# Optimization experiments

Measured on AMD Instinct MI355X. Metric: run time of the kernel, lower is better.

## Reference

```python
import jax, jax.numpy as jnp
import numpy as np

# Qwen3-Next gated delta-net dims
H_K, H_V, DK, DV = 16, 32, 128, 128
HID, KCONV = 2048, 4
KEY_DIM, VALUE_DIM = H_K * DK, H_V * DV      # 2048, 4096
CONV_DIM = 2 * KEY_DIM + VALUE_DIM           # 8192
GV = H_V // H_K                              # v-heads per k-head = 2
EPS = 1e-6
SEQ = 4096


def setup_inputs() -> dict:
    key = jax.random.key(0)
    ks = jax.random.split(key, 8)
    n = lambda k, sh, s: jax.random.normal(k, sh, jnp.float32) * s
    return {
        "hidden_states": n(ks[0], (SEQ, HID), 1.0),
        "W_qkvz": n(ks[1], (HID, 2 * KEY_DIM + 2 * VALUE_DIM), HID ** -0.5),
        "W_ba": n(ks[2], (HID, 2 * H_V), HID ** -0.5),
        "conv_w": n(ks[3], (CONV_DIM, KCONV), 0.5),
        "A_log": jnp.log(jax.random.uniform(ks[4], (H_V,), jnp.float32, 1.0, 16.0)),
        "dt_bias": jnp.ones((H_V,), jnp.float32),
        "norm_weight": jnp.ones((DV,), jnp.float32),
        "W_out": n(ks[5], (VALUE_DIM, HID), VALUE_DIM ** -0.5),
    }


def _l2norm(x):
    return x * jax.lax.rsqrt(jnp.sum(x * x, -1, keepdims=True) + EPS)


def reference(hidden_states, W_qkvz, W_ba, conv_w, A_log, dt_bias, norm_weight, W_out):
    L = hidden_states.shape[0]
    # 1. input projections
    qkvz = hidden_states @ W_qkvz            # (L, 12288)
    ba = hidden_states @ W_ba                # (L, 64)
    # fix_query_key_value_ordering: view per k-head group then split
    qkvz = qkvz.reshape(L, H_K, 2 * DK + 2 * GV * DV)
    q = qkvz[:, :, :DK]                                         # (L, Hk, dk)
    k = qkvz[:, :, DK:2 * DK]                                   # (L, Hk, dk)
    v = qkvz[:, :, 2 * DK:2 * DK + GV * DV].reshape(L, H_V, DV)  # (L, Hv, dv)
    z = qkvz[:, :, 2 * DK + GV * DV:].reshape(L, H_V, DV)
    ba = ba.reshape(L, H_K, 2 * GV)
    b = ba[:, :, :GV].reshape(L, H_V)
    a = ba[:, :, GV:].reshape(L, H_V)

    # 2. causal depthwise conv1d over [q|k|v] channels + silu
    mixed = jnp.concatenate([q.reshape(L, KEY_DIM), k.reshape(L, KEY_DIM),
                             v.reshape(L, VALUE_DIM)], axis=-1)  # (L, CONV_DIM)
    xp = jnp.pad(mixed, ((KCONV - 1, 0), (0, 0)))
    conv = sum(xp[i:i + L] * conv_w[:, i] for i in range(KCONV))
    mixed = jax.nn.silu(conv)

    q = mixed[:, :KEY_DIM].reshape(L, H_K, DK)
    k = mixed[:, KEY_DIM:2 * KEY_DIM].reshape(L, H_K, DK)
    v = mixed[:, 2 * KEY_DIM:].reshape(L, H_V, DV)

    # 3. fused gating: g = -exp(A_log) * softplus(a + dt_bias); beta = sigmoid(b)
    g = -jnp.exp(A_log) * jax.nn.softplus(a + dt_bias)   # (L, Hv)
    beta = jax.nn.sigmoid(b)                              # (L, Hv)

    # qk l2-norm + scale, expand k-heads to v-heads (GQA repeat)
    q = jnp.repeat(_l2norm(q), GV, axis=1) * (DK ** -0.5)  # (L, Hv, dk)
    k = jnp.repeat(_l2norm(k), GV, axis=1)

    # 4. gated delta-rule recurrence over time (state per head: dk x dv)
    def step(S, inp):
        qt, kt, vt, gt, bt = inp
        S = S * jnp.exp(gt)[:, None, None]
        kv = jnp.einsum('hkv,hk->hv', S, kt)
        delta = (vt - kv) * bt[:, None]
        S = S + kt[:, :, None] * delta[:, None, :]
        return S, jnp.einsum('hkv,hk->hv', S, qt)

    S0 = jnp.zeros((H_V, DK, DV), jnp.float32)
    _, core = jax.lax.scan(step, S0, (q, k, v, g, beta))   # (L, Hv, dv)

    # 5. gated RMSNorm (norm before gate): rmsnorm(x)*w * silu(z)
    var = jnp.mean(core * core, -1, keepdims=True)
    core = core * jax.lax.rsqrt(var + EPS) * norm_weight
    core = core * jax.nn.silu(z)

    # 6. output projection
    return core.reshape(L, VALUE_DIM) @ W_out
```

## Files before the change

### kernel.cpp

```cpp
#include <hip/hip_runtime.h>
#include <hip/hip_bf16.h>

#define SEQ 4096
#define HID 2048
#define HK_ 16
#define HV_ 32
#define KEY_DIM 2048
#define VALUE_DIM 4096
#define CONV_DIM 8192
#define NQKVZ 12288

typedef unsigned short ushort_t;
typedef short bf16x8 __attribute__((ext_vector_type(8)));
typedef float f32x4 __attribute__((ext_vector_type(4)));
typedef float f32x2 __attribute__((ext_vector_type(2)));

__device__ __forceinline__ float bf2f(ushort_t h) {
    union { unsigned int u; float f; } x; x.u = ((unsigned int)h) << 16; return x.f;
}
__device__ __forceinline__ void cvt8(uint4 v, float* f) {
    unsigned int w[4] = {v.x, v.y, v.z, v.w};
#pragma unroll
    for (int i = 0; i < 4; i++) {
        union { unsigned int u; float f; } lo, hi;
        lo.u = w[i] << 16; hi.u = w[i] & 0xffff0000u;
        f[2 * i] = lo.f; f[2 * i + 1] = hi.f;
    }
}
__device__ __forceinline__ void cvt8v(uint4 v, f32x2* f) {
    unsigned int w[4] = {v.x, v.y, v.z, v.w};
#pragma unroll
    for (int i = 0; i < 4; i++) {
        union { unsigned int u; float f; } lo, hi;
        lo.u = w[i] << 16; hi.u = w[i] & 0xffff0000u;
        f[i] = (f32x2){lo.f, hi.f};
    }
}
__device__ __forceinline__ ushort_t f2bf(float f) {
    union { float f; unsigned int u; } x; x.f = f;
    unsigned int u = x.u;
    u += 0x7fffu + ((u >> 16) & 1u);
    return (ushort_t)(u >> 16);
}

template <int CTRL>
__device__ __forceinline__ float dpp_add(float x) {
    union { float f; int i; } a, b;
    a.f = x;
    b.i = __builtin_amdgcn_update_dpp(0, a.i, CTRL, 0xF, 0xF, true);
    return a.f + b.f;
}
__device__ __forceinline__ float red16(float x) {
    x = dpp_add<0xB1>(x);
    x = dpp_add<0x4E>(x);
    x = dpp_add<0x141>(x);
    x = dpp_add<0x140>(x);
    return x;
}

__global__ void k_cvt(const float* __restrict__ src, ushort_t* __restrict__ dst)
{
    size_t i = ((size_t)blockIdx.x * 256 + threadIdx.x) * 8;
    float4 a = *(const float4*)&src[i];
    float4 b = *(const float4*)&src[i + 4];
    ushort_t u[8];
    u[0]=f2bf(a.x); u[1]=f2bf(a.y); u[2]=f2bf(a.z); u[3]=f2bf(a.w);
    u[4]=f2bf(b.x); u[5]=f2bf(b.y); u[6]=f2bf(b.z); u[7]=f2bf(b.w);
    *(uint4*)&dst[i] = *(uint4*)u;
}

__global__ __launch_bounds__(256) void k_transpose(const float* __restrict__ src,
                                                   ushort_t* __restrict__ dst,
                                                   int R, int C)
{
    __shared__ float tile[64][65];
    int c0 = blockIdx.x * 64, r0 = blockIdx.y * 64;
    int t = threadIdx.x;
    int tr = t >> 4, tc = (t & 15) * 4;
#pragma unroll
    for (int r = 0; r < 4; r++) {
        float4 v = *(const float4*)&src[(size_t)(r0 + tr + r * 16) * C + c0 + tc];
        tile[tr + r * 16][tc + 0] = v.x;
        tile[tr + r * 16][tc + 1] = v.y;
        tile[tr + r * 16][tc + 2] = v.z;
        tile[tr + r * 16][tc + 3] = v.w;
    }
    __syncthreads();
#pragma unroll
    for (int r = 0; r < 4; r++) {
        int n = c0 + tr + r * 16;
        ushort_t u[4];
#pragma unroll
        for (int i = 0; i < 4; i++) u[i] = f2bf(tile[tc + i][tr + r * 16]);
        *(uint2*)&dst[(size_t)n * R + r0 + tc] = *(uint2*)u;
    }
}

__global__ void k_ba(const float* __restrict__ A, const float* __restrict__ B,
                     const float* __restrict__ A_log, const float* __restrict__ dt_bias,
                     float* __restrict__ gbf)
{
    __shared__ float As[16][132];
    __shared__ float Bs[16][68];
    int tid = threadIdx.x;
    int m0 = blockIdx.x * 128;
    int tx = tid & 15, ty = tid >> 4;
    int arow = tid >> 2, akq = tid & 3;
    int brow = tid >> 4, bc4 = tid & 15;
    float acc[8][4];
#pragma unroll
    for (int i = 0; i < 8; i++)
#pragma unroll
        for (int j = 0; j < 4; j++) acc[i][j] = 0.f;

    for (int k0 = 0; k0 < HID; k0 += 16) {
        float4 a0 = *(const float4*)&A[(size_t)(m0 + arow) * HID + k0 + akq * 4];
        float4 a1 = *(const float4*)&A[(size_t)(m0 + arow + 64) * HID + k0 + akq * 4];
        float4 b0 = *(const float4*)&B[(size_t)(k0 + brow) * 64 + bc4 * 4];
        __syncthreads();
        As[akq * 4 + 0][arow] = a0.x; As[akq * 4 + 1][arow] = a0.y;
        As[akq * 4 + 2][arow] = a0.z; As[akq * 4 + 3][arow] = a0.w;
        As[akq * 4 + 0][arow + 64] = a1.x; As[akq * 4 + 1][arow + 64] = a1.y;
        As[akq * 4 + 2][arow + 64] = a1.z; As[akq * 4 + 3][arow + 64] = a1.w;
        *(float4*)&Bs[brow][bc4 * 4] = b0;
        __syncthreads();
#pragma unroll
        for (int kk = 0; kk < 16; kk++) {
            float xa[8], yb[4];
            *(float4*)&xa[0] = *(const float4*)&As[kk][ty * 8];
            *(float4*)&xa[4] = *(const float4*)&As[kk][ty * 8 + 4];
            *(float4*)&yb[0] = *(const float4*)&Bs[kk][tx * 4];
#pragma unroll
            for (int i = 0; i < 8; i++)
#pragma unroll
                for (int j = 0; j < 4; j++) acc[i][j] += xa[i] * yb[j];
        }
    }
#pragma unroll
    for (int i = 0; i < 8; i++) {
        int t = m0 + ty * 8 + i;
#pragma unroll
        for (int j = 0; j < 4; j++) {
            int c = tx * 4 + j;
            int hk = c >> 2, rr = c & 3;
            float val = acc[i][j];
            if (rr < 2) {
                int hv = hk * 2 + rr;
                gbf[(t * HV_ + hv) * 2 + 1] = 1.f / (1.f + expf(-val));
            } else {
                int hv = hk * 2 + (rr - 2);
                float v2 = val + dt_bias[hv];
                float sp = (v2 > 20.f) ? v2 : log1pf(expf(v2));
                float g = -expf(A_log[hv]) * sp;
                gbf[(t * HV_ + hv) * 2 + 0] = expf(g);
            }
        }
    }
}

__global__ __launch_bounds__(256) void k_gemm_qkvz(const ushort_t* __restrict__ Ab,
                                                   const ushort_t* __restrict__ Bt,
                                                   ushort_t* __restrict__ preact,
                                                   ushort_t* __restrict__ zb)
{
    __shared__ ushort_t As[128][40];
    __shared__ ushort_t Bs[128][40];
    int tid = threadIdx.x;
    int m0 = blockIdx.y * 128, n0 = blockIdx.x * 128;
    int lane = tid & 63, wave = tid >> 6;
    int wm = (wave >> 1) * 64, wn = (wave & 1) * 64;
    int quad = lane >> 4, l16 = lane & 15;
    int sr = tid >> 1, sh = tid & 1;

    f32x4 acc[4][4];
#pragma unroll
    for (int i = 0; i < 4; i++)
#pragma unroll
        for (int j = 0; j < 4; j++) acc[i][j] = (f32x4){0.f, 0.f, 0.f, 0.f};

    for (int k0 = 0; k0 < HID; k0 += 32) {
        uint4 av0 = *(const uint4*)&Ab[(size_t)(m0 + sr) * HID + k0 + sh * 16];
        uint4 av1 = *(const uint4*)&Ab[(size_t)(m0 + sr) * HID + k0 + sh * 16 + 8];
        uint4 bv0 = *(const uint4*)&Bt[(size_t)(n0 + sr) * HID + k0 + sh * 16];
        uint4 bv1 = *(const uint4*)&Bt[(size_t)(n0 + sr) * HID + k0 + sh * 16 + 8];
        __syncthreads();
        *(uint4*)&As[sr][sh * 16]     = av0;
        *(uint4*)&As[sr][sh * 16 + 8] = av1;
        *(uint4*)&Bs[sr][sh * 16]     = bv0;
        *(uint4*)&Bs[sr][sh * 16 + 8] = bv1;
        __syncthreads();
        bf16x8 af[4], bfr[4];
#pragma unroll
        for (int i = 0; i < 4; i++) af[i]  = *(bf16x8*)&As[wm + i * 16 + l16][quad * 8];
#pragma unroll
        for (int j = 0; j < 4; j++) bfr[j] = *(bf16x8*)&Bs[wn + j * 16 + l16][quad * 8];
#pragma unroll
        for (int i = 0; i < 4; i++)
#pragma unroll
            for (int j = 0; j < 4; j++)
                acc[i][j] = __builtin_amdgcn_mfma_f32_16x16x32_bf16(af[i], bfr[j], acc[i][j], 0, 0, 0);
    }
    int hk = n0 / 768, r = n0 % 768;
    ushort_t* dst; int ldd;
    if (r < 128)      { dst = preact + hk * 128;                    ldd = CONV_DIM; }
    else if (r < 256) { dst = preact + 2048 + hk * 128;             ldd = CONV_DIM; }
    else if (r < 512) { dst = preact + 4096 + hk * 256 + (r - 256); ldd = CONV_DIM; }
    else              { dst = zb + hk * 256 + (r - 512);            ldd = VALUE_DIM; }
#pragma unroll
    for (int i = 0; i < 4; i++)
#pragma unroll
        for (int j = 0; j < 4; j++)
#pragma unroll
            for (int rg = 0; rg < 4; rg++) {
                int m = m0 + wm + i * 16 + quad * 4 + rg;
                int n = wn + j * 16 + l16;
                dst[(size_t)m * ldd + n] = f2bf(acc[i][j][rg]);
            }
}

__global__ __launch_bounds__(256) void k_gemm_out(const ushort_t* __restrict__ Ab,
                                                  const ushort_t* __restrict__ Bt,
                                                  float* __restrict__ C)
{
    __shared__ ushort_t As[128][40];
    __shared__ ushort_t Bs[128][40];
    int tid = threadIdx.x;
    int m0 = blockIdx.y * 128, n0 = blockIdx.x * 128;
    int lane = tid & 63, wave = tid >> 6;
    int wm = (wave >> 1) * 64, wn = (wave & 1) * 64;
    int quad = lane >> 4, l16 = lane & 15;
    int sr = tid >> 1, sh = tid & 1;

    f32x4 acc[4][4];
#pragma unroll
    for (int i = 0; i < 4; i++)
#pragma unroll
        for (int j = 0; j < 4; j++) acc[i][j] = (f32x4){0.f, 0.f, 0.f, 0.f};

    for (int k0 = 0; k0 < VALUE_DIM; k0 += 32) {
        uint4 av0 = *(const uint4*)&Ab[(size_t)(m0 + sr) * VALUE_DIM + k0 + sh * 16];
        uint4 av1 = *(const uint4*)&Ab[(size_t)(m0 + sr) * VALUE_DIM + k0 + sh * 16 + 8];
        uint4 bv0 = *(const uint4*)&Bt[(size_t)(n0 + sr) * VALUE_DIM + k0 + sh * 16];
        uint4 bv1 = *(const uint4*)&Bt[(size_t)(n0 + sr) * VALUE_DIM + k0 + sh * 16 + 8];
        __syncthreads();
        *(uint4*)&As[sr][sh * 16]     = av0;
        *(uint4*)&As[sr][sh * 16 + 8] = av1;
        *(uint4*)&Bs[sr][sh * 16]     = bv0;
        *(uint4*)&Bs[sr][sh * 16 + 8] = bv1;
        __syncthreads();
        bf16x8 af[4], bfr[4];
#pragma unroll
        for (int i = 0; i < 4; i++) af[i]  = *(bf16x8*)&As[wm + i * 16 + l16][quad * 8];
#pragma unroll
        for (int j = 0; j < 4; j++) bfr[j] = *(bf16x8*)&Bs[wn + j * 16 + l16][quad * 8];
#pragma unroll
        for (int i = 0; i < 4; i++)
#pragma unroll
            for (int j = 0; j < 4; j++)
                acc[i][j] = __builtin_amdgcn_mfma_f32_16x16x32_bf16(af[i], bfr[j], acc[i][j], 0, 0, 0);
    }
#pragma unroll
    for (int i = 0; i < 4; i++)
#pragma unroll
        for (int j = 0; j < 4; j++)
#pragma unroll
            for (int rg = 0; rg < 4; rg++) {
                int m = m0 + wm + i * 16 + quad * 4 + rg;
                int n = n0 + wn + j * 16 + l16;
                C[(size_t)m * HID + n] = acc[i][j][rg];
            }
}

__global__ void k_conv(const ushort_t* __restrict__ pre, const float* __restrict__ cw,
                       ushort_t* __restrict__ qn, ushort_t* __restrict__ kn,
                       ushort_t* __restrict__ vv)
{
    __shared__ float red[4][2];
    int s = blockIdx.x;
    int t0 = blockIdx.y * 4;
    int d = threadIdx.x;
    int c = s * 128 + d;
    float w[4];
    *(float4*)w = *(const float4*)&cw[(size_t)c * 4];
    float p[7];
#pragma unroll
    for (int i = 0; i < 7; i++) {
        int tt = t0 + i - 3;
        p[i] = (tt >= 0) ? bf2f(pre[(size_t)tt * CONV_DIM + c]) : 0.f;
    }
    float x[4];
#pragma unroll
    for (int u = 0; u < 4; u++) {
        float a = p[u] * w[0] + p[u + 1] * w[1] + p[u + 2] * w[2] + p[u + 3] * w[3];
        x[u] = a / (1.f + expf(-a));
    }
    if (s < 32) {
        int wv = d >> 6, ln = d & 63;
#pragma unroll
        for (int u = 0; u < 4; u++) {
            float ss = x[u] * x[u];
            for (int m = 32; m >= 1; m >>= 1) ss += __shfl_xor(ss, m, 64);
            if (ln == 0) red[u][wv] = ss;
        }
        __syncthreads();
#pragma unroll
        for (int u = 0; u < 4; u++) {
            float tot = red[u][0] + red[u][1];
            float scale = 1.f / sqrtf(tot + 1e-6f);
            float val = x[u] * scale;
            int t = t0 + u;
            if (s < 16) qn[(size_t)t * KEY_DIM + s * 128 + d] = f2bf(val * 0.08838834764831845f);
            else        kn[(size_t)t * KEY_DIM + (s - 16) * 128 + d] = f2bf(val);
        }
    } else {
#pragma unroll
        for (int u = 0; u < 4; u++)
            vv[(size_t)(t0 + u) * VALUE_DIM + (s - 32) * 128 + d] = f2bf(x[u]);
    }
}

__device__ __forceinline__ void recur_step(f32x2 S[4],
    uint4& rk, uint4& rq, ushort_t& rv, float2& rgb,
    const ushort_t* kp, const ushort_t* qp, const ushort_t* vp,
    const float2* gb, int h, int tpre, float* outp, bool lead)
{
    f32x2 k2[4], q2[4];
    cvt8v(rk, k2);
    cvt8v(rq, q2);
    float v_ = bf2f(rv);
    float e = rgb.x, b = rgb.y;
    rk = *(const uint4*)(kp + (size_t)tpre * KEY_DIM);
    rq = *(const uint4*)(qp + (size_t)tpre * KEY_DIM);
    rv = vp[(size_t)tpre * VALUE_DIM];
    rgb = gb[tpre * HV_ + h];

    f32x2 acc = S[0] * k2[0];
    acc += S[1] * k2[1];
    acc += S[2] * k2[2];
    acc += S[3] * k2[3];
    float d1 = red16(acc.x + acc.y);
    float dl = (v_ - e * d1) * b;
    f32x2 e2  = (f32x2){e, e};
    f32x2 dl2 = (f32x2){dl, dl};
    f32x2 oacc = (f32x2){0.f, 0.f};
#pragma unroll
    for (int j = 0; j < 4; j++) {
        S[j] = S[j] * e2 + k2[j] * dl2;
        oacc += S[j] * q2[j];
    }
    float o = red16(oacc.x + oacc.y);
    if (lead) *outp = o;
}

__global__ __launch_bounds__(256) void k_recur(const ushort_t* __restrict__ qn,
                                               const ushort_t* __restrict__ kn,
                                               const ushort_t* __restrict__ vv,
                                               const float2* __restrict__ gb,
                                               float* __restrict__ core)
{
    int h = blockIdx.y;
    int hk = h >> 1;
    int kc = threadIdx.x & 15;
    int cl = threadIdx.x >> 4;
    int col = blockIdx.x * 16 + cl;
    int kqoff = hk * 128 + kc * 8;
    bool lead = (kc == 0);

    const ushort_t* kp = kn + kqoff;
    const ushort_t* qp = qn + kqoff;
    const ushort_t* vp = vv + h * 128 + col;
    float* outp = core + h * 128 + col;

    f32x2 S[4];
#pragma unroll
    for (int j = 0; j < 4; j++) S[j] = (f32x2){0.f, 0.f};

    uint4 rka = *(const uint4*)kp;
    uint4 rqa = *(const uint4*)qp;
    ushort_t rva = vp[0];
    float2 gba = gb[h];
    uint4 rkb = *(const uint4*)(kp + KEY_DIM);
    uint4 rqb = *(const uint4*)(qp + KEY_DIM);
    ushort_t rvb = vp[VALUE_DIM];
    float2 gbb = gb[HV_ + h];
    uint4 rkc = *(const uint4*)(kp + 2 * KEY_DIM);
    uint4 rqc = *(const uint4*)(qp + 2 * KEY_DIM);
    ushort_t rvc = vp[2 * VALUE_DIM];
    float2 gbc = gb[2 * HV_ + h];
    uint4 rkd = *(const uint4*)(kp + 3 * KEY_DIM);
    uint4 rqd = *(const uint4*)(qp + 3 * KEY_DIM);
    ushort_t rvd = vp[3 * VALUE_DIM];
    float2 gbd = gb[3 * HV_ + h];

    for (int t = 0; t < SEQ; t += 4) {
        int p0 = (t + 4 < SEQ) ? t + 4 : SEQ - 1;
        int p1 = (t + 5 < SEQ) ? t + 5 : SEQ - 1;
        int p2 = (t + 6 < SEQ) ? t + 6 : SEQ - 1;
        int p3 = (t + 7 < SEQ) ? t + 7 : SEQ - 1;
        recur_step(S, rka, rqa, rva, gba, kp, qp, vp, gb, h, p0,
                   outp + (size_t)t * VALUE_DIM, lead);
        recur_step(S, rkb, rqb, rvb, gbb, kp, qp, vp, gb, h, p1,
                   outp + (size_t)(t + 1) * VALUE_DIM, lead);
        recur_step(S, rkc, rqc, rvc, gbc, kp, qp, vp, gb, h, p2,
                   outp + (size_t)(t + 2) * VALUE_DIM, lead);
        recur_step(S, rkd, rqd, rvd, gbd, kp, qp, vp, gb, h, p3,
                   outp + (size_t)(t + 3) * VALUE_DIM, lead);
    }
}

__global__ void k_gate(const float* __restrict__ core, const ushort_t* __restrict__ z,
                       const float* __restrict__ nw, ushort_t* __restrict__ corebf)
{
    __shared__ float red[2];
    int hv = blockIdx.x, t = blockIdx.y, d = threadIdx.x;
    size_t idx = (size_t)t * VALUE_DIM + hv * 128 + d;
    float cval = core[idx];
    float ss = cval * cval;
    for (int m = 32; m >= 1; m >>= 1) ss += __shfl_xor(ss, m, 64);
    int wv = d >> 6, ln = d & 63;
    if (ln == 0) red[wv] = ss;
    __syncthreads();
    float var = (red[0] + red[1]) * (1.f / 128.f);
    float zv = bf2f(z[idx]);
    float out = cval * (1.f / sqrtf(var + 1e-6f)) * nw[d] * (zv / (1.f + expf(-zv)));
    corebf[idx] = f2bf(out);
}

extern "C" void kernel_launch(void* const* d_in, const int* in_sizes, int n_in,
                              void* d_out, int out_size, void* d_ws, size_t ws_size,
                              hipStream_t stream)
{
    const float* hs    = (const float*)d_in[0];
    const float* Wqkvz = (const float*)d_in[1];
    const float* Wba   = (const float*)d_in[2];
    const float* convw = (const float*)d_in[3];
    const float* Alog  = (const float*)d_in[4];
    const float* dtb   = (const float*)d_in[5];
    const float* nw    = (const float*)d_in[6];
    const float* Wout  = (const float*)d_in[7];
    float* out = (float*)d_out;

    char* w = (char*)d_ws;
    ushort_t* preact = (ushort_t*)w;
    float*    coreb  = (float*)w;
    w += (size_t)SEQ * CONV_DIM * 2;
    ushort_t* zb = (ushort_t*)w;  w += (size_t)SEQ * VALUE_DIM * 2;
    float* gbf   = (float*)w;     w += (size_t)SEQ * HV_ * 8;
    ushort_t* qnb = (ushort_t*)w; w += (size_t)SEQ * KEY_DIM * 2;
    ushort_t* knb = (ushort_t*)w; w += (size_t)SEQ * KEY_DIM * 2;
    ushort_t* vvb = (ushort_t*)w; w += (size_t)SEQ * VALUE_DIM * 2;
    size_t needed = (size_t)(w - (char*)d_ws);
    if (ws_size < needed) return;

    ushort_t* wqT    = qnb;
    ushort_t* hsb    = qnb + (size_t)24 * 1024 * 1024;
    ushort_t* woutT  = vvb;
    ushort_t* corebf = qnb;

    hipLaunchKernelGGL(k_ba, dim3(32), dim3(256), 0, stream, hs, Wba, Alog, dtb, gbf);
    hipLaunchKernelGGL(k_cvt, dim3(4096), dim3(256), 0, stream, hs, hsb);
    hipLaunchKernelGGL(k_transpose, dim3(192, 32), dim3(256), 0, stream, Wqkvz, wqT, HID, NQKVZ);
    hipLaunchKernelGGL(k_gemm_qkvz, dim3(96, 32), dim3(256), 0, stream, hsb, wqT, preact, zb);
    hipLaunchKernelGGL(k_conv, dim3(64, 1024), dim3(128), 0, stream, preact, convw, qnb, knb, vvb);
    hipLaunchKernelGGL(k_recur, dim3(8, 32), dim3(256), 0, stream, qnb, knb, vvb,
                       (const float2*)gbf, coreb);
    hipLaunchKernelGGL(k_transpose, dim3(32, 64), dim3(256), 0, stream, Wout, woutT, VALUE_DIM, HID);
    hipLaunchKernelGGL(k_gate, dim3(32, 4096), dim3(128), 0, stream, coreb, zb, nw, corebf);
    hipLaunchKernelGGL(k_gemm_out, dim3(16, 32), dim3(256), 0, stream, corebf, woutT, out);
}
```

Before: 1.812 ms.

## Use direct global-to-LDS loads in GEMMs, vectorize conv, simplify recur prefetch

Both GEMM kernels now stage A/B tiles with global_load_lds, which writes straight into unpadded LDS instead of going through registers, and add a trailing barrier per k-step. The conv kernel is rewritten so each thread handles 8 channels with 128-bit loads and stores, using a DPP 16-lane reduction for the q/k l2-norm in place of shuffles plus shared memory. The recurrence prefetch index math is simplified to one clamped base per 4-step group. The cost is GEMM loads that are no longer software-pipelined, LDS tiles without padding that may bank-conflict on the fragment reads, and an extra sync per iteration.

Result: faster. 1.764 ms (-2.7%).

```diff
diff --git a/kernel.cpp b/kernel.cpp
--- a/kernel.cpp
+++ b/kernel.cpp
@@ -41,6 +41,12 @@
     unsigned int u = x.u;
     u += 0x7fffu + ((u >> 16) & 1u);
     return (ushort_t)(u >> 16);
+}
+
+__device__ __forceinline__ void gload_lds16(const void* g, void* l) {
+    __builtin_amdgcn_global_load_lds(
+        (const __attribute__((address_space(1))) void*)g,
+        (__attribute__((address_space(3))) void*)l, 16, 0, 0);
 }
 
 template <int CTRL>
@@ -163,14 +169,20 @@
                                                    ushort_t* __restrict__ preact,
                                                    ushort_t* __restrict__ zb)
 {
-    __shared__ ushort_t As[128][40];
-    __shared__ ushort_t Bs[128][40];
+    __shared__ ushort_t As[128][32];
+    __shared__ ushort_t Bs[128][32];
     int tid = threadIdx.x;
     int m0 = blockIdx.y * 128, n0 = blockIdx.x * 128;
     int lane = tid & 63, wave = tid >> 6;
     int wm = (wave >> 1) * 64, wn = (wave & 1) * 64;
     int quad = lane >> 4, l16 = lane & 15;
-    int sr = tid >> 1, sh = tid & 1;
+
+    int srow = ((wave & 1) << 6) + (lane >> 2);
+    int scol = (lane & 3) << 3;
+    const ushort_t* gsrc = (wave < 2)
+        ? &Ab[(size_t)(m0 + srow) * HID + scol]
+        : &Bt[(size_t)(n0 + srow) * HID + scol];
+    ushort_t* lbase = ((wave < 2) ? &As[0][0] : &Bs[0][0]) + ((wave & 1) << 11);
 
     f32x4 acc[4][4];
 #pragma unroll
@@ -179,15 +191,9 @@
         for (int j = 0; j < 4; j++) acc[i][j] = (f32x4){0.f, 0.f, 0.f, 0.f};
 
     for (int k0 = 0; k0 < HID; k0 += 32) {
-        uint4 av0 = *(const uint4*)&Ab[(size_t)(m0 + sr) * HID + k0 + sh * 16];
-        uint4 av1 = *(const uint4*)&Ab[(size_t)(m0 + sr) * HID + k0 + sh * 16 + 8];
-        uint4 bv0 = *(const uint4*)&Bt[(size_t)(n0 + sr) * HID + k0 + sh * 16];
-        uint4 bv1 = *(const uint4*)&Bt[(size_t)(n0 + sr) * HID + k0 + sh * 16 + 8];
-        __syncthreads();
-        *(uint4*)&As[sr][sh * 16]     = av0;
-        *(uint4*)&As[sr][sh * 16 + 8] = av1;
-        *(uint4*)&Bs[sr][sh * 16]     = bv0;
-        *(uint4*)&Bs[sr][sh * 16 + 8] = bv1;
+#pragma unroll
+        for (int i = 0; i < 4; i++)
+            gload_lds16(gsrc + k0 + (size_t)i * 16 * HID, lbase + i * 512);
         __syncthreads();
         bf16x8 af[4], bfr[4];
 #pragma unroll
@@ -199,6 +205,7 @@
 #pragma unroll
             for (int j = 0; j < 4; j++)
                 acc[i][j] = __builtin_amdgcn_mfma_f32_16x16x32_bf16(af[i], bfr[j], acc[i][j], 0, 0, 0);
+        __syncthreads();
     }
     int hk = n0 / 768, r = n0 % 768;
     ushort_t* dst; int ldd;
@@ -222,14 +229,20 @@
                                                   const ushort_t* __restrict__ Bt,
                                                   float* __restrict__ C)
 {
-    __shared__ ushort_t As[128][40];
-    __shared__ ushort_t Bs[128][40];
+    __shared__ ushort_t As[128][32];
+    __shared__ ushort_t Bs[128][32];
     int tid = threadIdx.x;
     int m0 = blockIdx.y * 128, n0 = blockIdx.x * 128;
     int lane = tid & 63, wave = tid >> 6;
     int wm = (wave >> 1) * 64, wn = (wave & 1) * 64;
     int quad = lane >> 4, l16 = lane & 15;
-    int sr = tid >> 1, sh = tid & 1;
+
+    int srow = ((wave & 1) << 6) + (lane >> 2);
+    int scol = (lane & 3) << 3;
+    const ushort_t* gsrc = (wave < 2)
+        ? &Ab[(size_t)(m0 + srow) * VALUE_DIM + scol]
+        : &Bt[(size_t)(n0 + srow) * VALUE_DIM + scol];
+    ushort_t* lbase = ((wave < 2) ? &As[0][0] : &Bs[0][0]) + ((wave & 1) << 11);
 
     f32x4 acc[4][4];
 #pragma unroll
@@ -238,15 +251,9 @@
         for (int j = 0; j < 4; j++) acc[i][j] = (f32x4){0.f, 0.f, 0.f, 0.f};
 
     for (int k0 = 0; k0 < VALUE_DIM; k0 += 32) {
-        uint4 av0 = *(const uint4*)&Ab[(size_t)(m0 + sr) * VALUE_DIM + k0 + sh * 16];
-        uint4 av1 = *(const uint4*)&Ab[(size_t)(m0 + sr) * VALUE_DIM + k0 + sh * 16 + 8];
-        uint4 bv0 = *(const uint4*)&Bt[(size_t)(n0 + sr) * VALUE_DIM + k0 + sh * 16];
-        uint4 bv1 = *(const uint4*)&Bt[(size_t)(n0 + sr) * VALUE_DIM + k0 + sh * 16 + 8];
-        __syncthreads();
-        *(uint4*)&As[sr][sh * 16]     = av0;
-        *(uint4*)&As[sr][sh * 16 + 8] = av1;
-        *(uint4*)&Bs[sr][sh * 16]     = bv0;
-        *(uint4*)&Bs[sr][sh * 16 + 8] = bv1;
+#pragma unroll
+        for (int i = 0; i < 4; i++)
+            gload_lds16(gsrc + k0 + (size_t)i * 16 * VALUE_DIM, lbase + i * 512);
         __syncthreads();
         bf16x8 af[4], bfr[4];
 #pragma unroll
@@ -258,6 +265,7 @@
 #pragma unroll
             for (int j = 0; j < 4; j++)
                 acc[i][j] = __builtin_amdgcn_mfma_f32_16x16x32_bf16(af[i], bfr[j], acc[i][j], 0, 0, 0);
+        __syncthreads();
     }
 #pragma unroll
     for (int i = 0; i < 4; i++)
@@ -271,51 +279,66 @@
             }
 }
 
-__global__ void k_conv(const ushort_t* __restrict__ pre, const float* __restrict__ cw,
-                       ushort_t* __restrict__ qn, ushort_t* __restrict__ kn,
-                       ushort_t* __restrict__ vv)
-{
-    __shared__ float red[4][2];
-    int s = blockIdx.x;
+__global__ __launch_bounds__(256) void k_conv(const ushort_t* __restrict__ pre,
+                                              const float* __restrict__ cw,
+                                              ushort_t* __restrict__ qn,
+                                              ushort_t* __restrict__ kn,
+                                              ushort_t* __restrict__ vv)
+{
+    int tid = threadIdx.x;
+    int c = blockIdx.x * 2048 + tid * 8;
     int t0 = blockIdx.y * 4;
-    int d = threadIdx.x;
-    int c = s * 128 + d;
-    float w[4];
-    *(float4*)w = *(const float4*)&cw[(size_t)c * 4];
-    float p[7];
+    float w[8][4];
+#pragma unroll
+    for (int j = 0; j < 8; j++)
+        *(float4*)w[j] = *(const float4*)&cw[(size_t)(c + j) * 4];
+    float p[7][8];
 #pragma unroll
     for (int i = 0; i < 7; i++) {
         int tt = t0 + i - 3;
-        p[i] = (tt >= 0) ? bf2f(pre[(size_t)tt * CONV_DIM + c]) : 0.f;
-    }
-    float x[4];
-#pragma unroll
-    for (int u = 0; u < 4; u++) {
-        float a = p[u] * w[0] + p[u + 1] * w[1] + p[u + 2] * w[2] + p[u + 3] * w[3];
-        x[u] = a / (1.f + expf(-a));
-    }
-    if (s < 32) {
-        int wv = d >> 6, ln = d & 63;
+        if (tt >= 0) {
+            uint4 v = *(const uint4*)&pre[(size_t)tt * CONV_DIM + c];
+            cvt8(v, p[i]);
+        } else {
+#pragma unroll
+            for (int j = 0; j < 8; j++) p[i][j] = 0.f;
+        }
+    }
+    float x[4][8];
+#pragma unroll
+    for (int u = 0; u < 4; u++)
+#pragma unroll
+        for (int j = 0; j < 8; j++) {
+            float a = p[u][j] * w[j][0] + p[u + 1][j] * w[j][1]
+                    + p[u + 2][j] * w[j][2] + p[u + 3][j] * w[j][3];
+            x[u][j] = a / (1.f + expf(-a));
+        }
+    if (blockIdx.x < 2) {
+        bool isq = (blockIdx.x == 0);
+        float headscale = isq ? 0.08838834764831845f : 1.f;
+        ushort_t* dst = isq ? qn : kn;
+        int cc = isq ? c : (c - KEY_DIM);
 #pragma unroll
         for (int u = 0; u < 4; u++) {
-            float ss = x[u] * x[u];
-            for (int m = 32; m >= 1; m >>= 1) ss += __shfl_xor(ss, m, 64);
-            if (ln == 0) red[u][wv] = ss;
-        }
-        __syncthreads();
+            float ss = 0.f;
+#pragma unroll
+            for (int j = 0; j < 8; j++) ss += x[u][j] * x[u][j];
+            ss = red16(ss);
+            float mul = headscale / sqrtf(ss + 1e-6f);
+            ushort_t o[8];
+#pragma unroll
+            for (int j = 0; j < 8; j++) o[j] = f2bf(x[u][j] * mul);
+            *(uint4*)&dst[(size_t)(t0 + u) * KEY_DIM + cc] = *(uint4*)o;
+        }
+    } else {
+        int cc = c - 2 * KEY_DIM;
 #pragma unroll
         for (int u = 0; u < 4; u++) {
-            float tot = red[u][0] + red[u][1];
-            float scale = 1.f / sqrtf(tot + 1e-6f);
-            float val = x[u] * scale;
-            int t = t0 + u;
-            if (s < 16) qn[(size_t)t * KEY_DIM + s * 128 + d] = f2bf(val * 0.08838834764831845f);
-            else        kn[(size_t)t * KEY_DIM + (s - 16) * 128 + d] = f2bf(val);
-        }
-    } else {
-#pragma unroll
-        for (int u = 0; u < 4; u++)
-            vv[(size_t)(t0 + u) * VALUE_DIM + (s - 32) * 128 + d] = f2bf(x[u]);
+            ushort_t o[8];
+#pragma unroll
+            for (int j = 0; j < 8; j++) o[j] = f2bf(x[u][j]);
+            *(uint4*)&vv[(size_t)(t0 + u) * VALUE_DIM + cc] = *(uint4*)o;
+        }
     }
 }
 
@@ -393,17 +416,14 @@
     float2 gbd = gb[3 * HV_ + h];
 
     for (int t = 0; t < SEQ; t += 4) {
-        int p0 = (t + 4 < SEQ) ? t + 4 : SEQ - 1;
-        int p1 = (t + 5 < SEQ) ? t + 5 : SEQ - 1;
-        int p2 = (t + 6 < SEQ) ? t + 6 : SEQ - 1;
-        int p3 = (t + 7 < SEQ) ? t + 7 : SEQ - 1;
-        recur_step(S, rka, rqa, rva, gba, kp, qp, vp, gb, h, p0,
+        int tp = (t <= SEQ - 8) ? (t + 4) : t;
+        recur_step(S, rka, rqa, rva, gba, kp, qp, vp, gb, h, tp,
                    outp + (size_t)t * VALUE_DIM, lead);
-        recur_step(S, rkb, rqb, rvb, gbb, kp, qp, vp, gb, h, p1,
+        recur_step(S, rkb, rqb, rvb, gbb, kp, qp, vp, gb, h, tp + 1,
                    outp + (size_t)(t + 1) * VALUE_DIM, lead);
-        recur_step(S, rkc, rqc, rvc, gbc, kp, qp, vp, gb, h, p2,
+        recur_step(S, rkc, rqc, rvc, gbc, kp, qp, vp, gb, h, tp + 2,
                    outp + (size_t)(t + 2) * VALUE_DIM, lead);
-        recur_step(S, rkd, rqd, rvd, gbd, kp, qp, vp, gb, h, p3,
+        recur_step(S, rkd, rqd, rvd, gbd, kp, qp, vp, gb, h, tp + 3,
                    outp + (size_t)(t + 3) * VALUE_DIM, lead);
     }
 }
@@ -461,7 +481,7 @@
     hipLaunchKernelGGL(k_cvt, dim3(4096), dim3(256), 0, stream, hs, hsb);
     hipLaunchKernelGGL(k_transpose, dim3(192, 32), dim3(256), 0, stream, Wqkvz, wqT, HID, NQKVZ);
     hipLaunchKernelGGL(k_gemm_qkvz, dim3(96, 32), dim3(256), 0, stream, hsb, wqT, preact, zb);
-    hipLaunchKernelGGL(k_conv, dim3(64, 1024), dim3(128), 0, stream, preact, convw, qnb, knb, vvb);
+    hipLaunchKernelGGL(k_conv, dim3(4, 1024), dim3(256), 0, stream, preact, convw, qnb, knb, vvb);
     hipLaunchKernelGGL(k_recur, dim3(8, 32), dim3(256), 0, stream, qnb, knb, vvb,
                        (const float2*)gbf, coreb);
     hipLaunchKernelGGL(k_transpose, dim3(32, 64), dim3(256), 0, stream, Wout, woutT, VALUE_DIM, HID);
```
